# Kernel tuning notes

Hardware: AMD Instinct MI355X
Metric: run time of the kernel (lower is better)

Reference implementation:

```python
import jax, jax.numpy as jnp
import numpy as np

B, N, E = 32, 196, 1024          # batch, encoder tokens, encoder feature dim
D = 1024                          # decoder_token_size
V = 32000                         # vocab_size
T = 100                           # max_tokens_during_train
START = 0                         # start_token_id


def setup_inputs() -> dict:
    key = jax.random.key(0)
    ks = jax.random.split(key, 16)
    s = 0.02
    return {
        "features": jax.random.normal(ks[0], (B, N, E), jnp.float32),
        # features_attn_head: ReLU -> Linear(E, D)
        "W_fk": jax.random.normal(ks[1], (E, D), jnp.float32) * s,
        "b_fk": jnp.zeros((D,), jnp.float32),
        # features_values: ReLU -> Linear(E, D)
        "W_fv": jax.random.normal(ks[2], (E, D), jnp.float32) * s,
        "b_fv": jnp.zeros((D,), jnp.float32),
        # text_features_attn_head: ReLU -> Linear(D, D)
        "W_tk": jax.random.normal(ks[3], (D, D), jnp.float32) * s,
        "b_tk": jnp.zeros((D,), jnp.float32),
        # LSTMCell(D, D): gates ordered [i, f, g, o]
        "W_ih": jax.random.normal(ks[4], (D, 4 * D), jnp.float32) * s,
        "W_hh": jax.random.normal(ks[5], (D, 4 * D), jnp.float32) * s,
        "b_ih": jnp.zeros((4 * D,), jnp.float32),
        "b_hh": jnp.zeros((4 * D,), jnp.float32),
        # lm_head: Linear(D, V)
        "W_lm": jax.random.normal(ks[6], (D, V), jnp.float32) * s,
        "b_lm": jnp.zeros((V,), jnp.float32),
        # bos token embedding (text_embedding(start_token_id)), detached in fwd
        "bos_embed": jax.random.normal(ks[7], (D,), jnp.float32) * s,
    }


def reference(features, W_fk, b_fk, W_fv, b_fv, W_tk, b_tk,
              W_ih, W_hh, b_ih, b_hh, W_lm, b_lm, bos_embed):
    scale = jnp.sqrt(jnp.asarray(D, jnp.float32))
    # encoder-side projections (constant over decode steps)
    context_key = jax.nn.relu(features) @ W_fk + b_fk      # [B, N, D]
    context_values = jax.nn.relu(features) @ W_fv + b_fv   # [B, N, D]

    h0 = jnp.broadcast_to(jax.lax.stop_gradient(bos_embed)[None, :], (B, D))
    c0 = jnp.zeros((B, D), jnp.float32)

    def step(carry, _):
        h, c = carry
        # input_values = hidden_state.detach().clone()
        q_in = jax.lax.stop_gradient(h)
        seq_keys = jax.nn.relu(q_in) @ W_tk + b_tk          # [B, D]
        # scaled_dot_product_attention(context_key, seq_keys[:,None,:], context_values)
        dot = jnp.einsum('bnd,bd->bn', context_key, seq_keys)[..., None] / scale  # [B,N,1]
        attn = jax.nn.softmax(dot, axis=-1)                 # softmax over size-1 dim -> ones
        ctx = jnp.einsum('bn,bnd->bd', attn[..., 0], context_values)  # [B, D]
        # torch LSTMCell
        gates = ctx @ W_ih + h @ W_hh + b_ih + b_hh         # [B, 4D]
        i_, f_, g_, o_ = jnp.split(gates, 4, axis=-1)
        c_new = jax.nn.sigmoid(f_) * c + jax.nn.sigmoid(i_) * jnp.tanh(g_)
        h_new = jax.nn.sigmoid(o_) * jnp.tanh(c_new)
        logits = h_new @ W_lm + b_lm                        # [B, V]
        return (h_new, c_new), logits

    _, logits_seq = jax.lax.scan(step, (h0, c0), None, length=T - 1)  # [T-1, B, V]
    first = jnp.zeros((1, B, V), jnp.float32).at[0, :, START].set(1.0)
    return jnp.concatenate([first, logits_seq], axis=0)    # [T, B, V]
```

## Files before the change

### kernel.cpp

```cpp
#include <hip/hip_runtime.h>
#include <hip/hip_bf16.h>
#include <stdint.h>

typedef __attribute__((ext_vector_type(8))) short short8;
typedef __attribute__((ext_vector_type(4))) float f32x4;

#define B_ 32
#define N_ 196
#define D_ 1024
#define V_ 32000
#define NSTEP 99
#define MROWS 3168
#define MPAD  3200
#define SENT  0x7FC07FC07FC07FC0ULL

#define OFF_WT     0ULL
#define OFF_H      65536000ULL
#define OFF_FSUM   72089600ULL
#define OFF_CTXP   72220672ULL
#define OFF_GBASEP 72482816ULL

#define AS3 __attribute__((address_space(3)))
#define AS1 __attribute__((address_space(1)))
static __device__ __forceinline__ void gload_lds16(const void* g, void* l) {
  __builtin_amdgcn_global_load_lds((const AS1 uint32_t*)g, (AS3 uint32_t*)l, 16, 0, 0);
}

__global__ void k_fsum(const float* __restrict__ feat, float* __restrict__ fsum,
                       unsigned long long* __restrict__ Hq) {
  if (blockIdx.x >= 128) {
    int gid = (blockIdx.x - 128) * 256 + threadIdx.x;
    for (int w = gid; w < NSTEP * 8192; w += 65536) Hq[w] = SENT;
    return;
  }
  int idx = blockIdx.x * 256 + threadIdx.x;
  int b = idx >> 10, e = idx & 1023;
  const float* p = feat + (size_t)b * (N_ * D_) + e;
  float s = 0.f;
  #pragma unroll 4
  for (int n = 0; n < N_; ++n) s += fmaxf(p[(size_t)n * D_], 0.f);
  fsum[idx] = s;
}

__global__ void k_ctx(const float* __restrict__ fsum, const float* __restrict__ W_fv,
                      const float* __restrict__ b_fv, float* __restrict__ ctxp) {
  __shared__ float fs[16][512];
  int kc = blockIdx.z;
  int e0 = kc * 512;
  int b0 = blockIdx.y * 16;
  int d = blockIdx.x * 64 + (threadIdx.x & 63);
  int bq = threadIdx.x >> 6;
  for (int i = threadIdx.x; i < 8192; i += 256)
    fs[i >> 9][i & 511] = fsum[(b0 + (i >> 9)) * 1024 + e0 + (i & 511)];
  __syncthreads();
  float bias = (kc == 0) ? 196.f * b_fv[d] : 0.f;
  float acc[4] = {bias, bias, bias, bias};
  for (int e4 = 0; e4 < 128; ++e4) {
    float w0 = W_fv[(size_t)(e0 + 4 * e4 + 0) * 1024 + d];
    float w1 = W_fv[(size_t)(e0 + 4 * e4 + 1) * 1024 + d];
    float w2 = W_fv[(size_t)(e0 + 4 * e4 + 2) * 1024 + d];
    float w3 = W_fv[(size_t)(e0 + 4 * e4 + 3) * 1024 + d];
    #pragma unroll
    for (int r = 0; r < 4; ++r) {
      float4 c = *(const float4*)&fs[bq * 4 + r][e4 * 4];
      acc[r] = fmaf(c.x, w0, fmaf(c.y, w1, fmaf(c.z, w2, fmaf(c.w, w3, acc[r]))));
    }
  }
  #pragma unroll
  for (int r = 0; r < 4; ++r)
    ctxp[kc * 32768 + (size_t)(b0 + bq * 4 + r) * 1024 + d] = acc[r];
}

__global__ void k_gbase(const float* __restrict__ ctxp, const float* __restrict__ W_ih,
                        const float* __restrict__ b_ih, const float* __restrict__ b_hh,
                        float* __restrict__ gbasep) {
  __shared__ float cs[16][256];
  int kc = blockIdx.z;
  int e0 = kc * 256;
  int b0 = blockIdx.y * 16;
  int j = blockIdx.x * 256 + threadIdx.x;
  for (int i = threadIdx.x; i < 4096; i += 256) {
    int r = i >> 8, e = i & 255;
    cs[r][e] = ctxp[(size_t)(b0 + r) * 1024 + e0 + e]
             + ctxp[32768 + (size_t)(b0 + r) * 1024 + e0 + e];
  }
  __syncthreads();
  float bias = (kc == 0) ? (b_ih[j] + b_hh[j]) : 0.f;
  float acc[16];
  #pragma unroll
  for (int r = 0; r < 16; ++r) acc[r] = bias;
  for (int e4 = 0; e4 < 64; ++e4) {
    float w0 = W_ih[(size_t)(e0 + 4 * e4 + 0) * 4096 + j];
    float w1 = W_ih[(size_t)(e0 + 4 * e4 + 1) * 4096 + j];
    float w2 = W_ih[(size_t)(e0 + 4 * e4 + 2) * 4096 + j];
    float w3 = W_ih[(size_t)(e0 + 4 * e4 + 3) * 4096 + j];
    #pragma unroll
    for (int r = 0; r < 16; ++r) {
      float4 c = *(const float4*)&cs[r][e4 * 4];
      acc[r] = fmaf(c.x, w0, fmaf(c.y, w1, fmaf(c.z, w2, fmaf(c.w, w3, acc[r]))));
    }
  }
  #pragma unroll
  for (int r = 0; r < 16; ++r)
    gbasep[kc * 131072 + (size_t)(b0 + r) * 4096 + j] = acc[r];
}

__global__ __launch_bounds__(256, 1) void k_rec(
    const float* __restrict__ gbasep, const float* __restrict__ W_hh,
    const float* __restrict__ bos, unsigned long long* __restrict__ Hq,
    const float* __restrict__ W_lm, __hip_bfloat16* __restrict__ WT,
    float* __restrict__ out) {
  extern __shared__ char lds[];
  const int tid = threadIdx.x;
  const int blk = blockIdx.x;

  if (blk >= 128) {
    __hip_bfloat16* t = (__hip_bfloat16*)lds;
    int wblk = blk - 128;
    for (int idx = wblk * 256 + tid; idx < B_ * V_; idx += 128 * 256)
      __builtin_nontemporal_store(((idx % V_) == 0) ? 1.0f : 0.0f, &out[idx]);
    if (wblk < 64) ((uint32_t*)(Hq + (size_t)MROWS * 256))[wblk * 256 + tid] = 0u;
    int tx = tid & 63, ty = tid >> 6;
    int word = tx & 31, nh = tx >> 5;
    for (int tile = wblk; tile < 8000; tile += 128) {
      int k0 = (tile & 15) * 64;
      int n0 = (tile >> 4) * 64;
      __syncthreads();
      #pragma unroll
      for (int i = 0; i < 16; ++i) {
        int r = i * 4 + ty;
        t[r * 66 + tx] = __float2bfloat16(
            __builtin_nontemporal_load(&W_lm[(size_t)(k0 + r) * V_ + n0 + tx]));
      }
      __syncthreads();
      #pragma unroll
      for (int i = 0; i < 8; ++i) {
        int n = i * 8 + ty * 2 + nh;
        uint32_t lo = *(const uint16_t*)&t[2 * word * 66 + n];
        uint32_t hi = *(const uint16_t*)&t[(2 * word + 1) * 66 + n];
        __builtin_nontemporal_store(lo | (hi << 16),
            (uint32_t*)&WT[(size_t)(n0 + n) * 1024 + k0] + word);
      }
    }
    return;
  }

  __hip_bfloat16* hbuf = (__hip_bfloat16*)lds;
  __hip_bfloat16* wbuf = (__hip_bfloat16*)(lds + 32768);
  float* gex = (float*)(lds + 32768);

  const int bh = blk >> 6;
  const int dg = blk & 63;

  for (int idx = tid; idx < 64 * 1024; idx += 256) {
    int c = idx & 63;
    int k = idx >> 6;
    float w = W_hh[(size_t)k * 4096 + (c >> 4) * 1024 + dg * 16 + (c & 15)];
    wbuf[c * 1024 + ((((k >> 3) ^ (c & 7)) << 3) | (k & 7))] = __float2bfloat16(w);
  }
  for (int idx = tid; idx < 16 * 1024; idx += 256) {
    int row = idx >> 10;
    int k = idx & 1023;
    hbuf[row * 1024 + ((((k >> 3) ^ (row & 7)) << 3) | (k & 7))] = __float2bfloat16(bos[k]);
  }

  const int btl = tid >> 4;
  const int dl = tid & 15;
  float gb0 = 0.f, gb1 = 0.f, gb2 = 0.f, gb3 = 0.f;
  #pragma unroll
  for (int kc = 0; kc < 4; ++kc) {
    size_t base = (size_t)kc * 131072 + (size_t)(bh * 16 + btl) * 4096 + dg * 16 + dl;
    gb0 += gbasep[base + 0 * 1024];
    gb1 += gbasep[base + 1 * 1024];
    gb2 += gbasep[base + 2 * 1024];
    gb3 += gbasep[base + 3 * 1024];
  }
  float cst = 0.f;

  const int lane = tid & 63;
  const int wid = tid >> 6;
  const int arow = lane & 15;
  const int bcol = wid * 16 + (lane & 15);
  const int kg = lane >> 4;
  const int axor = arow & 7;

  __syncthreads();

  short8 breg[32];
  #pragma unroll
  for (int kt = 0; kt < 32; ++kt) {
    int ca = kt * 4 + kg;
    breg[kt] = *(const short8*)&wbuf[bcol * 1024 + ((ca ^ (bcol & 7)) << 3)];
  }

  const int pubw = (bh * 16 + btl) * 256 + dg * 4 + (dl >> 2);

  for (int t = 0; t < NSTEP; ++t) {
    f32x4 acc0 = {0.f, 0.f, 0.f, 0.f};
    f32x4 acc1 = {0.f, 0.f, 0.f, 0.f};
    #pragma unroll
    for (int kt = 0; kt < 32; kt += 2) {
      int ca = kt * 4 + kg;
      short8 a0 = *(const short8*)&hbuf[arow * 1024 + ((ca ^ axor) << 3)];
      acc0 = __builtin_amdgcn_mfma_f32_16x16x32_bf16(a0, breg[kt], acc0, 0, 0, 0);
      short8 a1 = *(const short8*)&hbuf[arow * 1024 + (((ca + 4) ^ axor) << 3)];
      acc1 = __builtin_amdgcn_mfma_f32_16x16x32_bf16(a1, breg[kt + 1], acc1, 0, 0, 0);
    }
    acc0 = acc0 + acc1;
    __syncthreads();
    {
      int bq = (lane >> 4) << 2;
      #pragma unroll
      for (int q = 0; q < 4; ++q) gex[(bq + q) * 68 + bcol] = acc0[q];
    }
    __syncthreads();

    float gi = gex[btl * 68 + 0  + dl] + gb0;
    float gf = gex[btl * 68 + 16 + dl] + gb1;
    float gg = gex[btl * 68 + 32 + dl] + gb2;
    float go = gex[btl * 68 + 48 + dl] + gb3;
    float si = 1.f / (1.f + __expf(-gi));
    float sf = 1.f / (1.f + __expf(-gf));
    float so = 1.f / (1.f + __expf(-go));
    cst = sf * cst + si * tanhf(gg);
    float h = so * tanhf(cst);

    float h1 = __shfl_down(h, 1);
    float h2 = __shfl_down(h, 2);
    float h3 = __shfl_down(h, 3);
    if ((dl & 3) == 0) {
      __hip_bfloat16 q0 = __float2bfloat16(h), q1 = __float2bfloat16(h1);
      __hip_bfloat16 q2 = __float2bfloat16(h2), q3 = __float2bfloat16(h3);
      unsigned long long v = (unsigned long long)*(uint16_t*)&q0
                           | ((unsigned long long)*(uint16_t*)&q1 << 16)
                           | ((unsigned long long)*(uint16_t*)&q2 << 32)
                           | ((unsigned long long)*(uint16_t*)&q3 << 48);
      __hip_atomic_store(&Hq[(size_t)t * 8192 + pubw], v,
                         __ATOMIC_RELAXED, __HIP_MEMORY_SCOPE_AGENT);
    }

    if (t == NSTEP - 1) break;

    {
      const unsigned long long* src = Hq + (size_t)t * 8192 + (size_t)bh * 16 * 256;
      for (;;) {
        unsigned long long v[16];
        #pragma unroll
        for (int j = 0; j < 16; ++j)
          v[j] = __hip_atomic_load(&src[j * 256 + tid],
                                   __ATOMIC_RELAXED, __HIP_MEMORY_SCOPE_AGENT);
        int nready = 0;
        #pragma unroll
        for (int j = 0; j < 16; ++j) {
          if (v[j] != SENT) {
            int off = (((tid >> 1) ^ (j & 7)) << 3) + ((tid & 1) << 2);
            *(uint2*)&hbuf[j * 1024 + off] = *(uint2*)&v[j];
            ++nready;
          }
        }
        if (nready == 16) break;
        __builtin_amdgcn_s_sleep(1);
      }
    }
    __syncthreads();
  }
}

__global__ __launch_bounds__(512, 1) void k_gemm(
    const __hip_bfloat16* __restrict__ H,
    const __hip_bfloat16* __restrict__ WT,
    const float* __restrict__ b_lm,
    float* __restrict__ out) {
  extern __shared__ char glds[];
  __hip_bfloat16* As = (__hip_bfloat16*)glds;
  __hip_bfloat16* Bs = (__hip_bfloat16*)(glds + 65536);

  int bid = blockIdx.x;
  int xcd = bid & 7;
  int idx = bid >> 3;
  int wg = (xcd < 1 ? xcd * 204 : 204 + (xcd - 1) * 203) + idx;
  int nt = wg / 13;
  int mt = wg - nt * 13;
  const int mbase = mt * 256;
  const int nbase = nt * 256;

  const int tid = threadIdx.x;
  const int lane = tid & 63;
  const int wid = tid >> 6;
  const int wm = wid >> 2;
  const int wn = wid & 3;

  f32x4 acc[8][4];
  #pragma unroll
  for (int m = 0; m < 8; ++m)
    #pragma unroll
    for (int n = 0; n < 4; ++n) acc[m][n] = (f32x4){0.f, 0.f, 0.f, 0.f};

  const int kg = lane >> 4;

  int srowA[4], srowB[4], soff[4];
  #pragma unroll
  for (int j = 0; j < 4; ++j) {
    int c = j * 512 + tid;
    int row = c >> 3;
    srowB[j] = nbase + row;
    srowA[j] = min(mbase + row, MPAD - 1);
    soff[j] = ((c & 7) ^ (row & 7)) * 8;
  }
  const int ldsbase = (tid & 448) * 8;

  auto STAGE = [&](int nb, int kt) {
    #pragma unroll
    for (int j = 0; j < 4; ++j)
      gload_lds16(H + (size_t)srowA[j] * 1024 + kt * 64 + soff[j],
                  As + nb * 16384 + j * 4096 + ldsbase);
    #pragma unroll
    for (int j = 0; j < 4; ++j)
      gload_lds16(WT + (size_t)srowB[j] * 1024 + kt * 64 + soff[j],
                  Bs + nb * 16384 + j * 4096 + ldsbase);
  };
  auto COMPUTE = [&](int nb) {
    __builtin_amdgcn_s_setprio(1);
    #pragma unroll
    for (int kk = 0; kk < 2; ++kk) {
      const int slot = kk * 4 + kg;
      short8 a[8], b[4];
      #pragma unroll
      for (int m = 0; m < 8; ++m) {
        int r = wm * 128 + m * 16 + (lane & 15);
        a[m] = *(const short8*)&As[nb * 16384 + r * 64 + ((slot ^ (r & 7)) << 3)];
      }
      #pragma unroll
      for (int n = 0; n < 4; ++n) {
        int r = wn * 64 + n * 16 + (lane & 15);
        b[n] = *(const short8*)&Bs[nb * 16384 + r * 64 + ((slot ^ (r & 7)) << 3)];
      }
      #pragma unroll
      for (int m = 0; m < 8; ++m)
        #pragma unroll
        for (int n = 0; n < 4; ++n)
          acc[m][n] = __builtin_amdgcn_mfma_f32_16x16x32_bf16(a[m], b[n], acc[m][n], 0, 0, 0);
    }
    __builtin_amdgcn_s_setprio(0);
  };

  STAGE(0, 0);
  asm volatile("s_waitcnt vmcnt(0)" ::: "memory");
  __builtin_amdgcn_s_barrier();
  for (int kt = 0; kt < 16; ++kt) {
    if (kt < 15) STAGE((kt + 1) & 1, kt + 1);
    COMPUTE(kt & 1);
    asm volatile("s_waitcnt vmcnt(0)" ::: "memory");
    __builtin_amdgcn_s_barrier();
  }

  if (mt != 12) {
    #pragma unroll
    for (int n = 0; n < 4; ++n) {
      int gcol = nbase + wn * 64 + n * 16 + (lane & 15);
      float bl = b_lm[gcol];
      #pragma unroll
      for (int m = 0; m < 8; ++m) {
        int rbase = mbase + wm * 128 + m * 16 + ((lane >> 4) << 2);
        #pragma unroll
        for (int q = 0; q < 4; ++q)
          __builtin_nontemporal_store(acc[m][n][q] + bl,
              &out[(size_t)(rbase + q + 32) * V_ + gcol]);
      }
    }
  } else {
    #pragma unroll
    for (int n = 0; n < 4; ++n) {
      int gcol = nbase + wn * 64 + n * 16 + (lane & 15);
      float bl = b_lm[gcol];
      #pragma unroll
      for (int m = 0; m < 8; ++m) {
        int rbase = mbase + wm * 128 + m * 16 + ((lane >> 4) << 2);
        #pragma unroll
        for (int q = 0; q < 4; ++q) {
          int r = rbase + q;
          if (r < MROWS)
            __builtin_nontemporal_store(acc[m][n][q] + bl,
                &out[(size_t)(r + 32) * V_ + gcol]);
        }
      }
    }
  }
}

extern "C" void kernel_launch(void* const* d_in, const int* in_sizes, int n_in,
                              void* d_out, int out_size, void* d_ws, size_t ws_size,
                              hipStream_t stream) {
  const float* features = (const float*)d_in[0];
  const float* W_fv = (const float*)d_in[3];
  const float* b_fv = (const float*)d_in[4];
  const float* W_ih = (const float*)d_in[7];
  const float* W_hh = (const float*)d_in[8];
  const float* b_ih = (const float*)d_in[9];
  const float* b_hh = (const float*)d_in[10];
  const float* W_lm = (const float*)d_in[11];
  const float* b_lm = (const float*)d_in[12];
  const float* bos  = (const float*)d_in[13];
  float* out = (float*)d_out;
  char* ws = (char*)d_ws;

  __hip_bfloat16* WT     = (__hip_bfloat16*)(ws + OFF_WT);
  __hip_bfloat16* H      = (__hip_bfloat16*)(ws + OFF_H);
  unsigned long long* Hq = (unsigned long long*)(ws + OFF_H);
  float* fsum            = (float*)(ws + OFF_FSUM);
  float* ctxp            = (float*)(ws + OFF_CTXP);
  float* gbasep          = (float*)(ws + OFF_GBASEP);

  hipLaunchKernelGGL(k_fsum,  dim3(384),       dim3(256), 0, stream, features, fsum, Hq);
  hipLaunchKernelGGL(k_ctx,   dim3(16, 2, 2),  dim3(256), 0, stream, fsum, W_fv, b_fv, ctxp);
  hipLaunchKernelGGL(k_gbase, dim3(16, 2, 4),  dim3(256), 0, stream, ctxp, W_ih, b_ih, b_hh, gbasep);
  hipLaunchKernelGGL(k_rec,   dim3(256),  dim3(256), 163840, stream,
                     gbasep, W_hh, bos, Hq, W_lm, WT, out);
  hipLaunchKernelGGL(k_gemm,  dim3(1625), dim3(512), 131072, stream, H, WT, b_lm, out);
}
```

Before: 758.2 us.

## Fuse LM-head GEMM into recurrent kernel with work-stealing tiles gated on step progress

Merges the separate LM-head GEMM into the recurrent kernel as a persistent phase. All blocks pull 256x128 output tiles from an atomic work counter, and each tile waits on per-batch-half step counters so logits for early timesteps are computed while the recurrence is still running. H tiles are read with atomic loads from the published hidden-state queue instead of a separate buffer, and blocks are widened to 512 threads so two can co-reside. This adds spin-waiting, a smaller GEMM tile with more tiles, and a risk of deadlock if the GEMM blocks starve the recurrent blocks.

New measurement: 786.7 us. 1.04x slower.

```diff
diff --git a/kernel.cpp b/kernel.cpp
--- a/kernel.cpp
+++ b/kernel.cpp
@@ -13,17 +13,22 @@
 #define MROWS 3168
 #define MPAD  3200
 #define SENT  0x7FC07FC07FC07FC0ULL
+#define NITEMS 3250
 
 #define OFF_WT     0ULL
 #define OFF_H      65536000ULL
 #define OFF_FSUM   72089600ULL
 #define OFF_CTXP   72220672ULL
 #define OFF_GBASEP 72482816ULL
+#define OFF_CTL    74579968ULL
 
 #define AS3 __attribute__((address_space(3)))
 #define AS1 __attribute__((address_space(1)))
 static __device__ __forceinline__ void gload_lds16(const void* g, void* l) {
   __builtin_amdgcn_global_load_lds((const AS1 uint32_t*)g, (AS3 uint32_t*)l, 16, 0, 0);
+}
+static __device__ __forceinline__ unsigned long long aload(const unsigned long long* p) {
+  return __hip_atomic_load(p, __ATOMIC_RELAXED, __HIP_MEMORY_SCOPE_AGENT);
 }
 
 __global__ void k_fsum(const float* __restrict__ feat, float* __restrict__ fsum,
@@ -105,21 +110,26 @@
     gbasep[kc * 131072 + (size_t)(b0 + r) * 4096 + j] = acc[r];
 }
 
-__global__ __launch_bounds__(256, 1) void k_rec(
+__global__ __launch_bounds__(512, 2) void k_rec(
     const float* __restrict__ gbasep, const float* __restrict__ W_hh,
     const float* __restrict__ bos, unsigned long long* __restrict__ Hq,
     const float* __restrict__ W_lm, __hip_bfloat16* __restrict__ WT,
-    float* __restrict__ out) {
+    const float* __restrict__ b_lm, float* __restrict__ out,
+    uint32_t* __restrict__ ctl) {
   extern __shared__ char lds[];
   const int tid = threadIdx.x;
   const int blk = blockIdx.x;
+  const int lane = tid & 63;
+  const int wid = tid >> 6;
 
   if (blk >= 128) {
     __hip_bfloat16* t = (__hip_bfloat16*)lds;
     int wblk = blk - 128;
-    for (int idx = wblk * 256 + tid; idx < B_ * V_; idx += 128 * 256)
+    for (int idx = wblk * 512 + tid; idx < B_ * V_; idx += 128 * 512)
       __builtin_nontemporal_store(((idx % V_) == 0) ? 1.0f : 0.0f, &out[idx]);
-    if (wblk < 64) ((uint32_t*)(Hq + (size_t)MROWS * 256))[wblk * 256 + tid] = 0u;
+    if (wblk < 16)
+      __hip_atomic_store(&Hq[(size_t)MROWS * 256 + wblk * 512 + tid], 0ULL,
+                         __ATOMIC_RELAXED, __HIP_MEMORY_SCOPE_AGENT);
     int tx = tid & 63, ty = tid >> 6;
     int word = tx & 31, nh = tx >> 5;
     for (int tile = wblk; tile < 8000; tile += 128) {
@@ -127,261 +137,327 @@
       int n0 = (tile >> 4) * 64;
       __syncthreads();
       #pragma unroll
-      for (int i = 0; i < 16; ++i) {
-        int r = i * 4 + ty;
+      for (int i = 0; i < 8; ++i) {
+        int r = i * 8 + ty;
         t[r * 66 + tx] = __float2bfloat16(
             __builtin_nontemporal_load(&W_lm[(size_t)(k0 + r) * V_ + n0 + tx]));
       }
       __syncthreads();
       #pragma unroll
-      for (int i = 0; i < 8; ++i) {
-        int n = i * 8 + ty * 2 + nh;
+      for (int i = 0; i < 4; ++i) {
+        int n = i * 16 + ty * 2 + nh;
         uint32_t lo = *(const uint16_t*)&t[2 * word * 66 + n];
         uint32_t hi = *(const uint16_t*)&t[(2 * word + 1) * 66 + n];
         __builtin_nontemporal_store(lo | (hi << 16),
             (uint32_t*)&WT[(size_t)(n0 + n) * 1024 + k0] + word);
       }
     }
-    return;
-  }
-
-  __hip_bfloat16* hbuf = (__hip_bfloat16*)lds;
-  __hip_bfloat16* wbuf = (__hip_bfloat16*)(lds + 32768);
-  float* gex = (float*)(lds + 32768);
-
-  const int bh = blk >> 6;
-  const int dg = blk & 63;
-
-  for (int idx = tid; idx < 64 * 1024; idx += 256) {
-    int c = idx & 63;
-    int k = idx >> 6;
-    float w = W_hh[(size_t)k * 4096 + (c >> 4) * 1024 + dg * 16 + (c & 15)];
-    wbuf[c * 1024 + ((((k >> 3) ^ (c & 7)) << 3) | (k & 7))] = __float2bfloat16(w);
-  }
-  for (int idx = tid; idx < 16 * 1024; idx += 256) {
-    int row = idx >> 10;
-    int k = idx & 1023;
-    hbuf[row * 1024 + ((((k >> 3) ^ (row & 7)) << 3) | (k & 7))] = __float2bfloat16(bos[k]);
-  }
-
-  const int btl = tid >> 4;
-  const int dl = tid & 15;
-  float gb0 = 0.f, gb1 = 0.f, gb2 = 0.f, gb3 = 0.f;
-  #pragma unroll
-  for (int kc = 0; kc < 4; ++kc) {
-    size_t base = (size_t)kc * 131072 + (size_t)(bh * 16 + btl) * 4096 + dg * 16 + dl;
-    gb0 += gbasep[base + 0 * 1024];
-    gb1 += gbasep[base + 1 * 1024];
-    gb2 += gbasep[base + 2 * 1024];
-    gb3 += gbasep[base + 3 * 1024];
-  }
-  float cst = 0.f;
-
-  const int lane = tid & 63;
-  const int wid = tid >> 6;
-  const int arow = lane & 15;
-  const int bcol = wid * 16 + (lane & 15);
-  const int kg = lane >> 4;
-  const int axor = arow & 7;
-
-  __syncthreads();
-
-  short8 breg[32];
-  #pragma unroll
-  for (int kt = 0; kt < 32; ++kt) {
-    int ca = kt * 4 + kg;
-    breg[kt] = *(const short8*)&wbuf[bcol * 1024 + ((ca ^ (bcol & 7)) << 3)];
-  }
-
-  const int pubw = (bh * 16 + btl) * 256 + dg * 4 + (dl >> 2);
-
-  for (int t = 0; t < NSTEP; ++t) {
-    f32x4 acc0 = {0.f, 0.f, 0.f, 0.f};
-    f32x4 acc1 = {0.f, 0.f, 0.f, 0.f};
+    asm volatile("s_waitcnt vmcnt(0)" ::: "memory");
+    __threadfence();
+    __syncthreads();
+    if (tid == 0) atomicAdd(&ctl[2], 1u);
+  } else {
+    __hip_bfloat16* hbuf = (__hip_bfloat16*)lds;
+    __hip_bfloat16* wbuf = (__hip_bfloat16*)(lds + 32768);
+    float* gex = (float*)(lds + 32768);
+
+    const int bh = blk >> 6;
+    const int dg = blk & 63;
+
+    for (int idx = tid; idx < 64 * 1024; idx += 512) {
+      int c = idx & 63;
+      int k = idx >> 6;
+      float w = W_hh[(size_t)k * 4096 + (c >> 4) * 1024 + dg * 16 + (c & 15)];
+      wbuf[c * 1024 + ((((k >> 3) ^ (c & 7)) << 3) | (k & 7))] = __float2bfloat16(w);
+    }
+    for (int idx = tid; idx < 16 * 1024; idx += 512) {
+      int row = idx >> 10;
+      int k = idx & 1023;
+      hbuf[row * 1024 + ((((k >> 3) ^ (row & 7)) << 3) | (k & 7))] = __float2bfloat16(bos[k]);
+    }
+
+    const int btl = tid >> 4;
+    const int dl = tid & 15;
+    float gb0 = 0.f, gb1 = 0.f, gb2 = 0.f, gb3 = 0.f;
+    if (tid < 256) {
+      #pragma unroll
+      for (int kc = 0; kc < 4; ++kc) {
+        size_t base = (size_t)kc * 131072 + (size_t)(bh * 16 + btl) * 4096 + dg * 16 + dl;
+        gb0 += gbasep[base + 0 * 1024];
+        gb1 += gbasep[base + 1 * 1024];
+        gb2 += gbasep[base + 2 * 1024];
+        gb3 += gbasep[base + 3 * 1024];
+      }
+    }
+    float cst = 0.f;
+
+    const int arow = lane & 15;
+    const int bcolr = (wid & 3) * 16 + (lane & 15);
+    const int kg = lane >> 4;
+    const int axor = arow & 7;
+
+    __syncthreads();
+
+    short8 breg[32];
     #pragma unroll
-    for (int kt = 0; kt < 32; kt += 2) {
+    for (int kt = 0; kt < 32; ++kt) {
       int ca = kt * 4 + kg;
-      short8 a0 = *(const short8*)&hbuf[arow * 1024 + ((ca ^ axor) << 3)];
-      acc0 = __builtin_amdgcn_mfma_f32_16x16x32_bf16(a0, breg[kt], acc0, 0, 0, 0);
-      short8 a1 = *(const short8*)&hbuf[arow * 1024 + (((ca + 4) ^ axor) << 3)];
-      acc1 = __builtin_amdgcn_mfma_f32_16x16x32_bf16(a1, breg[kt + 1], acc1, 0, 0, 0);
-    }
-    acc0 = acc0 + acc1;
+      breg[kt] = *(const short8*)&wbuf[bcolr * 1024 + ((ca ^ (bcolr & 7)) << 3)];
+    }
+
+    const int pubw = (bh * 16 + (btl & 15)) * 256 + dg * 4 + (dl >> 2);
+
+    for (int t = 0; t < NSTEP; ++t) {
+      f32x4 acc0 = {0.f, 0.f, 0.f, 0.f};
+      f32x4 acc1 = {0.f, 0.f, 0.f, 0.f};
+      if (wid < 4) {
+        #pragma unroll
+        for (int kt = 0; kt < 32; kt += 2) {
+          int ca = kt * 4 + kg;
+          short8 a0 = *(const short8*)&hbuf[arow * 1024 + ((ca ^ axor) << 3)];
+          acc0 = __builtin_amdgcn_mfma_f32_16x16x32_bf16(a0, breg[kt], acc0, 0, 0, 0);
+          short8 a1 = *(const short8*)&hbuf[arow * 1024 + (((ca + 4) ^ axor) << 3)];
+          acc1 = __builtin_amdgcn_mfma_f32_16x16x32_bf16(a1, breg[kt + 1], acc1, 0, 0, 0);
+        }
+        acc0 = acc0 + acc1;
+      }
+      __syncthreads();
+      if (wid < 4) {
+        int bq = (lane >> 4) << 2;
+        #pragma unroll
+        for (int q = 0; q < 4; ++q) gex[(bq + q) * 68 + bcolr] = acc0[q];
+      }
+      __syncthreads();
+
+      if (tid < 256) {
+        float gi = gex[btl * 68 + 0  + dl] + gb0;
+        float gf = gex[btl * 68 + 16 + dl] + gb1;
+        float gg = gex[btl * 68 + 32 + dl] + gb2;
+        float go = gex[btl * 68 + 48 + dl] + gb3;
+        float si = 1.f / (1.f + __expf(-gi));
+        float sf = 1.f / (1.f + __expf(-gf));
+        float so = 1.f / (1.f + __expf(-go));
+        cst = sf * cst + si * tanhf(gg);
+        float h = so * tanhf(cst);
+        float h1 = __shfl_down(h, 1);
+        float h2 = __shfl_down(h, 2);
+        float h3 = __shfl_down(h, 3);
+        if ((dl & 3) == 0) {
+          __hip_bfloat16 q0 = __float2bfloat16(h), q1 = __float2bfloat16(h1);
+          __hip_bfloat16 q2 = __float2bfloat16(h2), q3 = __float2bfloat16(h3);
+          unsigned long long v = (unsigned long long)*(uint16_t*)&q0
+                               | ((unsigned long long)*(uint16_t*)&q1 << 16)
+                               | ((unsigned long long)*(uint16_t*)&q2 << 32)
+                               | ((unsigned long long)*(uint16_t*)&q3 << 48);
+          __hip_atomic_store(&Hq[(size_t)t * 8192 + pubw], v,
+                             __ATOMIC_RELAXED, __HIP_MEMORY_SCOPE_AGENT);
+        }
+      }
+
+      if (t == NSTEP - 1) break;
+
+      {
+        const unsigned long long* src = Hq + (size_t)t * 8192 + (size_t)bh * 4096;
+        for (;;) {
+          unsigned long long v[8];
+          #pragma unroll
+          for (int j = 0; j < 8; ++j) v[j] = aload(&src[j * 512 + tid]);
+          int nready = 0;
+          #pragma unroll
+          for (int j = 0; j < 8; ++j) {
+            if (v[j] != SENT) {
+              int w = j * 512 + tid;
+              int row = w >> 8, c = w & 255;
+              int off = (((c >> 1) ^ (row & 7)) << 3) + ((c & 1) << 2);
+              *(uint2*)&hbuf[row * 1024 + off] = *(uint2*)&v[j];
+              ++nready;
+            }
+          }
+          if (nready == 8) break;
+          __builtin_amdgcn_s_sleep(1);
+        }
+      }
+      __syncthreads();
+      if (dg == 0 && tid == 0)
+        __hip_atomic_store(&ctl[bh], (uint32_t)(t + 1), __ATOMIC_RELAXED, __HIP_MEMORY_SCOPE_AGENT);
+    }
+
+    if (dg == 0) {
+      const unsigned long long* src = Hq + (size_t)98 * 8192 + (size_t)bh * 4096;
+      for (;;) {
+        int nready = 0;
+        #pragma unroll
+        for (int j = 0; j < 8; ++j)
+          if (aload(&src[j * 512 + tid]) != SENT) ++nready;
+        if (nready == 8) break;
+        __builtin_amdgcn_s_sleep(1);
+      }
+      __syncthreads();
+      if (tid == 0)
+        __hip_atomic_store(&ctl[bh], 1000u, __ATOMIC_RELAXED, __HIP_MEMORY_SCOPE_AGENT);
+    }
     __syncthreads();
-    {
-      int bq = (lane >> 4) << 2;
+  }
+
+  {
+    __hip_bfloat16* As = (__hip_bfloat16*)lds;
+    __hip_bfloat16* Bs = (__hip_bfloat16*)(lds + 65536);
+    volatile int* bc = (volatile int*)(lds + 98304);
+
+    if (tid == 0) {
+      while (__hip_atomic_load(&ctl[2], __ATOMIC_RELAXED, __HIP_MEMORY_SCOPE_AGENT) < 128u)
+        __builtin_amdgcn_s_sleep(8);
+    }
+    __syncthreads();
+    __threadfence();
+
+    const int wm = wid >> 1;
+    const int wn = wid & 1;
+    const int kg = lane >> 4;
+
+    int brr[2], bso[2];
+    #pragma unroll
+    for (int j = 0; j < 2; ++j) {
+      int c = j * 512 + tid;
+      int r = c >> 3;
+      brr[j] = r;
+      bso[j] = ((c & 7) ^ (r & 7)) * 8;
+    }
+    int alr[4], asl[4];
+    #pragma unroll
+    for (int j = 0; j < 4; ++j) {
+      int c = j * 512 + tid;
+      alr[j] = c >> 3;
+      asl[j] = c & 7;
+    }
+    const int ldsb = (tid & 448) * 8;
+
+    for (;;) {
+      if (tid == 0) *bc = (int)atomicAdd(&ctl[3], 1u);
+      __syncthreads();
+      int it = *bc;
+      __syncthreads();
+      if (it >= NITEMS) break;
+      int g = it / 250;
+      int nt = it - g * 250;
+      const int mbase = g * 256;
+      const int nbase = nt * 128;
+      uint32_t need = (uint32_t)(8 * g + 8 < 99 ? 8 * g + 8 : 99);
+      if (tid == 0) {
+        for (;;) {
+          uint32_t c0 = __hip_atomic_load(&ctl[0], __ATOMIC_RELAXED, __HIP_MEMORY_SCOPE_AGENT);
+          uint32_t c1 = __hip_atomic_load(&ctl[1], __ATOMIC_RELAXED, __HIP_MEMORY_SCOPE_AGENT);
+          if (c0 >= need && c1 >= need) break;
+          __builtin_amdgcn_s_sleep(16);
+        }
+      }
+      __syncthreads();
+
+      int agr[4];
       #pragma unroll
-      for (int q = 0; q < 4; ++q) gex[(bq + q) * 68 + bcol] = acc0[q];
-    }
-    __syncthreads();
-
-    float gi = gex[btl * 68 + 0  + dl] + gb0;
-    float gf = gex[btl * 68 + 16 + dl] + gb1;
-    float gg = gex[btl * 68 + 32 + dl] + gb2;
-    float go = gex[btl * 68 + 48 + dl] + gb3;
-    float si = 1.f / (1.f + __expf(-gi));
-    float sf = 1.f / (1.f + __expf(-gf));
-    float so = 1.f / (1.f + __expf(-go));
-    cst = sf * cst + si * tanhf(gg);
-    float h = so * tanhf(cst);
-
-    float h1 = __shfl_down(h, 1);
-    float h2 = __shfl_down(h, 2);
-    float h3 = __shfl_down(h, 3);
-    if ((dl & 3) == 0) {
-      __hip_bfloat16 q0 = __float2bfloat16(h), q1 = __float2bfloat16(h1);
-      __hip_bfloat16 q2 = __float2bfloat16(h2), q3 = __float2bfloat16(h3);
-      unsigned long long v = (unsigned long long)*(uint16_t*)&q0
-                           | ((unsigned long long)*(uint16_t*)&q1 << 16)
-                           | ((unsigned long long)*(uint16_t*)&q2 << 32)
-                           | ((unsigned long long)*(uint16_t*)&q3 << 48);
-      __hip_atomic_store(&Hq[(size_t)t * 8192 + pubw], v,
-                         __ATOMIC_RELAXED, __HIP_MEMORY_SCOPE_AGENT);
-    }
-
-    if (t == NSTEP - 1) break;
-
-    {
-      const unsigned long long* src = Hq + (size_t)t * 8192 + (size_t)bh * 16 * 256;
-      for (;;) {
-        unsigned long long v[16];
-        #pragma unroll
-        for (int j = 0; j < 16; ++j)
-          v[j] = __hip_atomic_load(&src[j * 256 + tid],
-                                   __ATOMIC_RELAXED, __HIP_MEMORY_SCOPE_AGENT);
-        int nready = 0;
-        #pragma unroll
-        for (int j = 0; j < 16; ++j) {
-          if (v[j] != SENT) {
-            int off = (((tid >> 1) ^ (j & 7)) << 3) + ((tid & 1) << 2);
-            *(uint2*)&hbuf[j * 1024 + off] = *(uint2*)&v[j];
-            ++nready;
+      for (int j = 0; j < 4; ++j) agr[j] = min(mbase + alr[j], MPAD - 1);
+
+      f32x4 acc[4][4];
+      #pragma unroll
+      for (int m = 0; m < 4; ++m)
+        #pragma unroll
+        for (int n = 0; n < 4; ++n) acc[m][n] = (f32x4){0.f, 0.f, 0.f, 0.f};
+
+      unsigned long long av[8];
+      auto SB = [&](int nb, int kt) {
+        #pragma unroll
+        for (int j = 0; j < 2; ++j)
+          gload_lds16(WT + (size_t)(nbase + brr[j]) * 1024 + kt * 64 + bso[j],
+                      Bs + nb * 8192 + j * 4096 + ldsb);
+      };
+      auto ALOAD = [&](int kt) {
+        #pragma unroll
+        for (int j = 0; j < 4; ++j) {
+          size_t gw = (size_t)agr[j] * 256 + kt * 16 + asl[j] * 2;
+          av[2 * j]     = aload(&Hq[gw]);
+          av[2 * j + 1] = aload(&Hq[gw + 1]);
+        }
+      };
+      auto AWRITE = [&](int nb) {
+        #pragma unroll
+        for (int j = 0; j < 4; ++j) {
+          uint4 w;
+          w.x = (uint32_t)av[2 * j];     w.y = (uint32_t)(av[2 * j] >> 32);
+          w.z = (uint32_t)av[2 * j + 1]; w.w = (uint32_t)(av[2 * j + 1] >> 32);
+          *(uint4*)&As[nb * 16384 + alr[j] * 64 + ((asl[j] ^ (alr[j] & 7)) << 3)] = w;
+        }
+      };
+      auto COMPUTE = [&](int nb) {
+        __builtin_amdgcn_s_setprio(1);
+        #pragma unroll
+        for (int kk = 0; kk < 2; ++kk) {
+          const int slot = kk * 4 + kg;
+          short8 a[4], b[4];
+          #pragma unroll
+          for (int m = 0; m < 4; ++m) {
+            int r = wm * 64 + m * 16 + (lane & 15);
+            a[m] = *(const short8*)&As[nb * 16384 + r * 64 + ((slot ^ (r & 7)) << 3)];
           }
-        }
-        if (nready == 16) break;
-        __builtin_amdgcn_s_sleep(1);
-      }
-    }
-    __syncthreads();
-  }
-}
-
-__global__ __launch_bounds__(512, 1) void k_gemm(
-    const __hip_bfloat16* __restrict__ H,
-    const __hip_bfloat16* __restrict__ WT,
-    const float* __restrict__ b_lm,
-    float* __restrict__ out) {
-  extern __shared__ char glds[];
-  __hip_bfloat16* As = (__hip_bfloat16*)glds;
-  __hip_bfloat16* Bs = (__hip_bfloat16*)(glds + 65536);
-
-  int bid = blockIdx.x;
-  int xcd = bid & 7;
-  int idx = bid >> 3;
-  int wg = (xcd < 1 ? xcd * 204 : 204 + (xcd - 1) * 203) + idx;
-  int nt = wg / 13;
-  int mt = wg - nt * 13;
-  const int mbase = mt * 256;
-  const int nbase = nt * 256;
-
-  const int tid = threadIdx.x;
-  const int lane = tid & 63;
-  const int wid = tid >> 6;
-  const int wm = wid >> 2;
-  const int wn = wid & 3;
-
-  f32x4 acc[8][4];
-  #pragma unroll
-  for (int m = 0; m < 8; ++m)
-    #pragma unroll
-    for (int n = 0; n < 4; ++n) acc[m][n] = (f32x4){0.f, 0.f, 0.f, 0.f};
-
-  const int kg = lane >> 4;
-
-  int srowA[4], srowB[4], soff[4];
-  #pragma unroll
-  for (int j = 0; j < 4; ++j) {
-    int c = j * 512 + tid;
-    int row = c >> 3;
-    srowB[j] = nbase + row;
-    srowA[j] = min(mbase + row, MPAD - 1);
-    soff[j] = ((c & 7) ^ (row & 7)) * 8;
-  }
-  const int ldsbase = (tid & 448) * 8;
-
-  auto STAGE = [&](int nb, int kt) {
-    #pragma unroll
-    for (int j = 0; j < 4; ++j)
-      gload_lds16(H + (size_t)srowA[j] * 1024 + kt * 64 + soff[j],
-                  As + nb * 16384 + j * 4096 + ldsbase);
-    #pragma unroll
-    for (int j = 0; j < 4; ++j)
-      gload_lds16(WT + (size_t)srowB[j] * 1024 + kt * 64 + soff[j],
-                  Bs + nb * 16384 + j * 4096 + ldsbase);
-  };
-  auto COMPUTE = [&](int nb) {
-    __builtin_amdgcn_s_setprio(1);
-    #pragma unroll
-    for (int kk = 0; kk < 2; ++kk) {
-      const int slot = kk * 4 + kg;
-      short8 a[8], b[4];
-      #pragma unroll
-      for (int m = 0; m < 8; ++m) {
-        int r = wm * 128 + m * 16 + (lane & 15);
-        a[m] = *(const short8*)&As[nb * 16384 + r * 64 + ((slot ^ (r & 7)) << 3)];
-      }
-      #pragma unroll
-      for (int n = 0; n < 4; ++n) {
-        int r = wn * 64 + n * 16 + (lane & 15);
-        b[n] = *(const short8*)&Bs[nb * 16384 + r * 64 + ((slot ^ (r & 7)) << 3)];
-      }
-      #pragma unroll
-      for (int m = 0; m < 8; ++m)
-        #pragma unroll
-        for (int n = 0; n < 4; ++n)
-          acc[m][n] = __builtin_amdgcn_mfma_f32_16x16x32_bf16(a[m], b[n], acc[m][n], 0, 0, 0);
-    }
-    __builtin_amdgcn_s_setprio(0);
-  };
-
-  STAGE(0, 0);
-  asm volatile("s_waitcnt vmcnt(0)" ::: "memory");
-  __builtin_amdgcn_s_barrier();
-  for (int kt = 0; kt < 16; ++kt) {
-    if (kt < 15) STAGE((kt + 1) & 1, kt + 1);
-    COMPUTE(kt & 1);
-    asm volatile("s_waitcnt vmcnt(0)" ::: "memory");
-    __builtin_amdgcn_s_barrier();
-  }
-
-  if (mt != 12) {
-    #pragma unroll
-    for (int n = 0; n < 4; ++n) {
-      int gcol = nbase + wn * 64 + n * 16 + (lane & 15);
-      float bl = b_lm[gcol];
-      #pragma unroll
-      for (int m = 0; m < 8; ++m) {
-        int rbase = mbase + wm * 128 + m * 16 + ((lane >> 4) << 2);
-        #pragma unroll
-        for (int q = 0; q < 4; ++q)
-          __builtin_nontemporal_store(acc[m][n][q] + bl,
-              &out[(size_t)(rbase + q + 32) * V_ + gcol]);
-      }
-    }
-  } else {
-    #pragma unroll
-    for (int n = 0; n < 4; ++n) {
-      int gcol = nbase + wn * 64 + n * 16 + (lane & 15);
-      float bl = b_lm[gcol];
-      #pragma unroll
-      for (int m = 0; m < 8; ++m) {
-        int rbase = mbase + wm * 128 + m * 16 + ((lane >> 4) << 2);
-        #pragma unroll
-        for (int q = 0; q < 4; ++q) {
-          int r = rbase + q;
-          if (r < MROWS)
-            __builtin_nontemporal_store(acc[m][n][q] + bl,
-                &out[(size_t)(r + 32) * V_ + gcol]);
+          #pragma unroll
+          for (int n = 0; n < 4; ++n) {
+            int r = wn * 64 + n * 16 + (lane & 15);
+            b[n] = *(const short8*)&Bs[nb * 8192 + r * 64 + ((slot ^ (r & 7)) << 3)];
+          }
+          #pragma unroll
+          for (int m = 0; m < 4; ++m)
+            #pragma unroll
+            for (int n = 0; n < 4; ++n)
+              acc[m][n] = __builtin_amdgcn_mfma_f32_16x16x32_bf16(a[m], b[n], acc[m][n], 0, 0, 0);
+        }
+        __builtin_amdgcn_s_setprio(0);
+      };
+
+      SB(0, 0);
+      ALOAD(0);
+      asm volatile("s_waitcnt vmcnt(0)" ::: "memory");
+      AWRITE(0);
+      asm volatile("s_waitcnt lgkmcnt(0)" ::: "memory");
+      __builtin_amdgcn_s_barrier();
+      for (int kt = 0; kt < 16; ++kt) {
+        int cur = kt & 1;
+        if (kt < 15) { SB(cur ^ 1, kt + 1); ALOAD(kt + 1); }
+        COMPUTE(cur);
+        asm volatile("s_waitcnt vmcnt(0)" ::: "memory");
+        if (kt < 15) AWRITE(cur ^ 1);
+        asm volatile("s_waitcnt lgkmcnt(0)" ::: "memory");
+        __builtin_amdgcn_s_barrier();
+      }
+
+      if (g != 12) {
+        #pragma unroll
+        for (int n = 0; n < 4; ++n) {
+          int gcol = nbase + wn * 64 + n * 16 + (lane & 15);
+          float bl = b_lm[gcol];
+          #pragma unroll
+          for (int m = 0; m < 4; ++m) {
+            int rbase = mbase + wm * 64 + m * 16 + ((lane >> 4) << 2);
+            #pragma unroll
+            for (int q = 0; q < 4; ++q)
+              __builtin_nontemporal_store(acc[m][n][q] + bl,
+                  &out[(size_t)(rbase + q + 32) * V_ + gcol]);
+          }
+        }
+      } else {
+        #pragma unroll
+        for (int n = 0; n < 4; ++n) {
+          int gcol = nbase + wn * 64 + n * 16 + (lane & 15);
+          float bl = b_lm[gcol];
+          #pragma unroll
+          for (int m = 0; m < 4; ++m) {
+            int rbase = mbase + wm * 64 + m * 16 + ((lane >> 4) << 2);
+            #pragma unroll
+            for (int q = 0; q < 4; ++q) {
+              int r = rbase + q;
+              if (r < MROWS)
+                __builtin_nontemporal_store(acc[m][n][q] + bl,
+                    &out[(size_t)(r + 32) * V_ + gcol]);
+            }
+          }
         }
       }
     }
@@ -405,16 +481,16 @@
   char* ws = (char*)d_ws;
 
   __hip_bfloat16* WT     = (__hip_bfloat16*)(ws + OFF_WT);
-  __hip_bfloat16* H      = (__hip_bfloat16*)(ws + OFF_H);
   unsigned long long* Hq = (unsigned long long*)(ws + OFF_H);
   float* fsum            = (float*)(ws + OFF_FSUM);
   float* ctxp            = (float*)(ws + OFF_CTXP);
   float* gbasep          = (float*)(ws + OFF_GBASEP);
+  uint32_t* ctl          = (uint32_t*)(ws + OFF_CTL);
 
   hipLaunchKernelGGL(k_fsum,  dim3(384),       dim3(256), 0, stream, features, fsum, Hq);
   hipLaunchKernelGGL(k_ctx,   dim3(16, 2, 2),  dim3(256), 0, stream, fsum, W_fv, b_fv, ctxp);
   hipLaunchKernelGGL(k_gbase, dim3(16, 2, 4),  dim3(256), 0, stream, ctxp, W_ih, b_ih, b_hh, gbasep);
-  hipLaunchKernelGGL(k_rec,   dim3(256),  dim3(256), 163840, stream,
-                     gbasep, W_hh, bos, Hq, W_lm, WT, out);
-  hipLaunchKernelGGL(k_gemm,  dim3(1625), dim3(512), 131072, stream, H, WT, b_lm, out);
-}
+  hipMemsetAsync(ctl, 0, 64, stream);
+  hipLaunchKernelGGL(k_rec,   dim3(256), dim3(512), 163840, stream,
+                     gbasep, W_hh, bos, Hq, W_lm, WT, b_lm, out, ctl);
+}
```
